# Kernel tuning notes

Measured on AMD Instinct MI355X. Metric: run time of the kernel, lower is better.

Reference implementation:

```python
import jax, jax.numpy as jnp
import numpy as np

N_NODES = 100000
N_EDGES = 800000
F_IN = 128
C_HID = 32
N_CLS = 16
K_HOPS = 3
CST = 1e-05


def setup_inputs() -> dict:
    key = jax.random.key(0)
    ks = jax.random.split(key, 12)
    node_feat = jax.random.normal(ks[0], (N_NODES, F_IN), dtype=jnp.float32)
    edge_index = jax.random.randint(ks[1], (2, N_EDGES), 0, N_NODES, dtype=jnp.int64)
    def lin(k, fan_in, fan_out):
        bound = 1.0 / np.sqrt(fan_in)
        kw, kb = jax.random.split(k)
        W = jax.random.uniform(kw, (fan_in, fan_out), minval=-bound, maxval=bound, dtype=jnp.float32)
        b = jax.random.uniform(kb, (fan_out,), minval=-bound, maxval=bound, dtype=jnp.float32)
        return W, b
    W_in, b_in = lin(ks[2], F_IN, C_HID)
    Wq, bq = lin(ks[3], C_HID, C_HID)
    Wk, bk = lin(ks[4], C_HID, C_HID)
    Wv, bv = lin(ks[5], C_HID, N_CLS)
    hopwise = jnp.ones((K_HOPS + 1,), dtype=jnp.float32)
    return {"node_feat": node_feat, "edge_index": edge_index,
            "W_in": W_in, "b_in": b_in, "Wq": Wq, "bq": bq,
            "Wk": Wk, "bk": bk, "Wv": Wv, "bv": bv, "hopwise": hopwise}


def reference(node_feat, edge_index, W_in, b_in, Wq, bq, Wk, bk, Wv, bv, hopwise):
    n = node_feat.shape[0]
    row, col = edge_index[0], edge_index[1]  # messages flow row -> col (PyG source_to_target)
    x = jax.nn.relu(node_feat @ W_in + b_in)            # [n, c]
    Q = 1.0 + jax.nn.elu(x @ Wq + bq)                    # [n, c]
    K = 1.0 + jax.nn.elu(x @ Wk + bk)                    # [n, c]
    V = x @ Wv + bv                                      # [n, d]
    M = jnp.einsum('ni,nj->nij', K, V)                   # [n, c, d]
    hidden = V * hopwise[0]
    for hop in range(K_HOPS):
        # scatter-sum aggregation over edges (aggr='add')
        M = jax.ops.segment_sum(M[row], col, num_segments=n)  # [n, c, d]
        K = jax.ops.segment_sum(K[row], col, num_segments=n)  # [n, c]
        H = jnp.einsum('ni,nij->nj', Q, M)               # [n, d]
        C = jnp.einsum('ni,ni->n', Q, K)[:, None] + CST  # [n, 1]
        hidden = hidden + hopwise[hop + 1] * (H / C)
    return hidden
```

## Files before the change

### kernel.cpp

```cpp
#include <hip/hip_runtime.h>
#include <math.h>

#define NN 100000
#define NE 800000
#define F_IN 128
#define CH 32
#define NC 16
#define CSTF 1e-5f
#define CAP 48

typedef float v2f __attribute__((ext_vector_type(2)));
typedef float v4f __attribute__((ext_vector_type(4)));
typedef short v8s __attribute__((ext_vector_type(8)));

__device__ __forceinline__ float bf_lo(unsigned int u) {
    unsigned int t = u << 16;
    return __builtin_bit_cast(float, t);
}
__device__ __forceinline__ float bf_hi(unsigned int u) {
    unsigned int t = u & 0xffff0000u;
    return __builtin_bit_cast(float, t);
}
__device__ __forceinline__ float bf_val(unsigned short v) {
    unsigned int t = ((unsigned int)v) << 16;
    return __builtin_bit_cast(float, t);
}
__device__ __forceinline__ v2f bf_pair(unsigned int u) {
    v2f r; r.x = bf_lo(u); r.y = bf_hi(u); return r;
}
__device__ __forceinline__ unsigned int bf_round(float a) {
    unsigned int ua = __builtin_bit_cast(unsigned int, a);
    return (ua + 0x7fffu + ((ua >> 16) & 1u)) >> 16;
}
__device__ __forceinline__ short bfq(float a) {
    unsigned int ua = __builtin_bit_cast(unsigned int, a);
    return (short)((ua + 0x8000u) >> 16);
}
__device__ __forceinline__ unsigned int bf_pack2(float a, float b) {
    return bf_round(a) | (bf_round(b) << 16);
}

__device__ __forceinline__ float cl448(float a) {
    return fminf(fmaxf(a, -448.f), 448.f);
}

__device__ __forceinline__ float elu1(float x) {
    return 1.f + ((x > 0.f) ? x : (expf(x) - 1.f));
}

__global__ void zero_kernel(int* __restrict__ p, int n) {
    int i = blockIdx.x * 256 + threadIdx.x;
    if (i < n) p[i] = 0;
}

__global__ void detect_kernel(const int* __restrict__ ei, int* __restrict__ mode) {
    __shared__ int any_nz;
    if (threadIdx.x == 0) any_nz = 0;
    __syncthreads();
    int nz = 0;
    for (int i = threadIdx.x; i < 4096; i += 256) nz |= (ei[2 * i + 1] != 0);
    if (nz) atomicOr(&any_nz, 1);
    __syncthreads();
    if (threadIdx.x == 0) *mode = any_nz ? 0 : 1;
}

__device__ __forceinline__ int get_row(const int* ei, int e, int m) {
    return m ? ei[2 * e] : ei[e];
}
__device__ __forceinline__ int get_col(const int* ei, int e, int m) {
    return m ? ei[2 * NE + 2 * e] : ei[NE + e];
}

__global__ void fillb_kernel(const int* __restrict__ ei, int* __restrict__ deg,
                             int* __restrict__ srcs, const int* __restrict__ mode) {
    int e = blockIdx.x * 256 + threadIdx.x;
    int m = *mode;
    if (e < NE) {
        int c = get_col(ei, e, m);
        int p = atomicAdd(&deg[c], 1);
        if (p < CAP) srcs[(size_t)c * CAP + p] = get_row(ei, e, m);
    }
}

__global__ __launch_bounds__(256) void phase1_kernel(
    const float* __restrict__ feat, const float* __restrict__ Win,
    const float* __restrict__ bin, const float* __restrict__ Wq,
    const float* __restrict__ bq, const float* __restrict__ Wk,
    const float* __restrict__ bk, const float* __restrict__ Wv,
    const float* __restrict__ bv, const float* __restrict__ hopwise,
    float* __restrict__ Qg, unsigned short* __restrict__ Kb,
    unsigned short* __restrict__ Vb, float* __restrict__ out)
{
    __shared__ float xs_all[4][16 * 36];

    int tid  = threadIdx.x;
    int wid  = tid >> 6;
    int lane = tid & 63;
    int q    = lane >> 4;
    int col  = lane & 15;
    int node0 = (blockIdx.x * 4 + wid) * 16;

    v8s wb[4][2];
#pragma unroll
    for (int kk = 0; kk < 4; ++kk)
#pragma unroll
        for (int t = 0; t < 2; ++t)
#pragma unroll
            for (int j = 0; j < 8; ++j)
                wb[kk][t][j] = (short)bf_round(Win[(kk * 32 + q * 8 + j) * CH + t * 16 + col]);

    v8s wq[2], wk[2], wv;
#pragma unroll
    for (int t = 0; t < 2; ++t)
#pragma unroll
        for (int j = 0; j < 8; ++j) {
            wq[t][j] = (short)bf_round(Wq[(q * 8 + j) * CH + t * 16 + col]);
            wk[t][j] = (short)bf_round(Wk[(q * 8 + j) * CH + t * 16 + col]);
        }
#pragma unroll
    for (int j = 0; j < 8; ++j)
        wv[j] = (short)bf_round(Wv[(q * 8 + j) * NC + col]);

    float bin0 = bin[col], bin1 = bin[col + 16];
    float bq0 = bq[col], bq1 = bq[col + 16];
    float bk0 = bk[col], bk1 = bk[col + 16];
    float bv0 = bv[col];
    float hw0 = hopwise[0];

    int nodeA = node0 + col;
    int nclamp = nodeA < NN ? nodeA : NN - 1;
    const float* fr = feat + (size_t)nclamp * F_IN + q * 8;

    v4f acc0 = {0.f, 0.f, 0.f, 0.f}, acc1 = {0.f, 0.f, 0.f, 0.f};
#pragma unroll
    for (int kk = 0; kk < 4; ++kk) {
        float4 a = *(const float4*)(fr + kk * 32);
        float4 b = *(const float4*)(fr + kk * 32 + 4);
        v8s af;
        af[0] = bfq(a.x); af[1] = bfq(a.y); af[2] = bfq(a.z); af[3] = bfq(a.w);
        af[4] = bfq(b.x); af[5] = bfq(b.y); af[6] = bfq(b.z); af[7] = bfq(b.w);
        acc0 = __builtin_amdgcn_mfma_f32_16x16x32_bf16(af, wb[kk][0], acc0, 0, 0, 0);
        acc1 = __builtin_amdgcn_mfma_f32_16x16x32_bf16(af, wb[kk][1], acc1, 0, 0, 0);
    }

    float* xs = xs_all[wid];
#pragma unroll
    for (int r = 0; r < 4; ++r) {
        xs[(q * 4 + r) * 36 + col]      = fmaxf(acc0[r] + bin0, 0.f);
        xs[(q * 4 + r) * 36 + col + 16] = fmaxf(acc1[r] + bin1, 0.f);
    }

    float4 xa = *(const float4*)&xs[col * 36 + q * 8];
    float4 xb = *(const float4*)&xs[col * 36 + q * 8 + 4];
    v8s xf;
    xf[0] = bfq(xa.x); xf[1] = bfq(xa.y); xf[2] = bfq(xa.z); xf[3] = bfq(xa.w);
    xf[4] = bfq(xb.x); xf[5] = bfq(xb.y); xf[6] = bfq(xb.z); xf[7] = bfq(xb.w);

    v4f aq0 = {0.f,0.f,0.f,0.f}, aq1 = {0.f,0.f,0.f,0.f};
    v4f ak0 = {0.f,0.f,0.f,0.f}, ak1 = {0.f,0.f,0.f,0.f};
    v4f av  = {0.f,0.f,0.f,0.f};
    aq0 = __builtin_amdgcn_mfma_f32_16x16x32_bf16(xf, wq[0], aq0, 0, 0, 0);
    aq1 = __builtin_amdgcn_mfma_f32_16x16x32_bf16(xf, wq[1], aq1, 0, 0, 0);
    ak0 = __builtin_amdgcn_mfma_f32_16x16x32_bf16(xf, wk[0], ak0, 0, 0, 0);
    ak1 = __builtin_amdgcn_mfma_f32_16x16x32_bf16(xf, wk[1], ak1, 0, 0, 0);
    av  = __builtin_amdgcn_mfma_f32_16x16x32_bf16(xf, wv,    av,  0, 0, 0);

#pragma unroll
    for (int r = 0; r < 4; ++r) {
        int nd = node0 + 4 * q + r;
        if (nd < NN) {
            float q0 = elu1(aq0[r] + bq0);
            float q1 = elu1(aq1[r] + bq1);
            float k0 = elu1(ak0[r] + bk0);
            float k1 = elu1(ak1[r] + bk1);
            float vv = av[r] + bv0;
            Qg[(size_t)nd * CH + col]      = q0;
            Qg[(size_t)nd * CH + col + 16] = q1;
            Kb[(size_t)nd * CH + col]      = (unsigned short)bf_round(k0);
            Kb[(size_t)nd * CH + col + 16] = (unsigned short)bf_round(k1);
            Vb[(size_t)nd * NC + col]      = (unsigned short)bf_round(vv);
            out[(size_t)nd * NC + col]     = hw0 * vv;
        }
    }
}

template<bool RANK1, bool WRITE>
__global__ __launch_bounds__(256) void hopB_kernel(
    const float* __restrict__ Qg, const unsigned short* __restrict__ Kb,
    const unsigned short* __restrict__ Vb, const unsigned char* __restrict__ Min,
    unsigned char* __restrict__ Mout, unsigned short* __restrict__ Kout,
    const int* __restrict__ deg, const int* __restrict__ srcs,
    const float* __restrict__ hopw, int hop, float* __restrict__ out)
{
    int tid  = threadIdx.x;
    int wid  = tid >> 6;
    int lane = tid & 63;
    int node = __builtin_amdgcn_readfirstlane(blockIdx.x * 4 + wid);
    int jB   = lane >> 2;
    int s4   = lane & 3;
    int cseg = s4 * 8;
    int c32  = lane & 31;

    v2f acc2[4];
#pragma unroll
    for (int t = 0; t < 4; ++t) { acc2[t].x = 0.f; acc2[t].y = 0.f; }
    v2f kagg2[4];
#pragma unroll
    for (int t = 0; t < 4; ++t) { kagg2[t].x = 0.f; kagg2[t].y = 0.f; }
    float kagg = 0.f;

    int d = deg[node];
    if (d > CAP) d = CAP;
    const int* sl = srcs + (size_t)node * CAP;
    int i = 0;

    if (RANK1) {
        for (; i + 3 < d; i += 4) {
            int s0 = sl[i], s1 = sl[i+1], s2 = sl[i+2], s3 = sl[i+3];
            uint4 kr0 = *(const uint4*)(Kb + (size_t)s0 * CH + cseg);
            uint4 kr1 = *(const uint4*)(Kb + (size_t)s1 * CH + cseg);
            uint4 kr2 = *(const uint4*)(Kb + (size_t)s2 * CH + cseg);
            uint4 kr3 = *(const uint4*)(Kb + (size_t)s3 * CH + cseg);
            float vj0 = bf_val(Vb[(size_t)s0 * NC + jB]);
            float vj1 = bf_val(Vb[(size_t)s1 * NC + jB]);
            float vj2 = bf_val(Vb[(size_t)s2 * NC + jB]);
            float vj3 = bf_val(Vb[(size_t)s3 * NC + jB]);
            v2f k;
            k = bf_pair(kr0.x); kagg2[0] += k; acc2[0] += k * vj0;
            k = bf_pair(kr0.y); kagg2[1] += k; acc2[1] += k * vj0;
            k = bf_pair(kr0.z); kagg2[2] += k; acc2[2] += k * vj0;
            k = bf_pair(kr0.w); kagg2[3] += k; acc2[3] += k * vj0;
            k = bf_pair(kr1.x); kagg2[0] += k; acc2[0] += k * vj1;
            k = bf_pair(kr1.y); kagg2[1] += k; acc2[1] += k * vj1;
            k = bf_pair(kr1.z); kagg2[2] += k; acc2[2] += k * vj1;
            k = bf_pair(kr1.w); kagg2[3] += k; acc2[3] += k * vj1;
            k = bf_pair(kr2.x); kagg2[0] += k; acc2[0] += k * vj2;
            k = bf_pair(kr2.y); kagg2[1] += k; acc2[1] += k * vj2;
            k = bf_pair(kr2.z); kagg2[2] += k; acc2[2] += k * vj2;
            k = bf_pair(kr2.w); kagg2[3] += k; acc2[3] += k * vj2;
            k = bf_pair(kr3.x); kagg2[0] += k; acc2[0] += k * vj3;
            k = bf_pair(kr3.y); kagg2[1] += k; acc2[1] += k * vj3;
            k = bf_pair(kr3.z); kagg2[2] += k; acc2[2] += k * vj3;
            k = bf_pair(kr3.w); kagg2[3] += k; acc2[3] += k * vj3;
        }
        for (; i < d; ++i) {
            int s0 = sl[i];
            uint4 kr0 = *(const uint4*)(Kb + (size_t)s0 * CH + cseg);
            float vj0 = bf_val(Vb[(size_t)s0 * NC + jB]);
            v2f k;
            k = bf_pair(kr0.x); kagg2[0] += k; acc2[0] += k * vj0;
            k = bf_pair(kr0.y); kagg2[1] += k; acc2[1] += k * vj0;
            k = bf_pair(kr0.z); kagg2[2] += k; acc2[2] += k * vj0;
            k = bf_pair(kr0.w); kagg2[3] += k; acc2[3] += k * vj0;
        }
    } else {
        for (; i + 3 < d; i += 4) {
            int s0 = sl[i], s1 = sl[i+1], s2 = sl[i+2], s3 = sl[i+3];
            uint2 u0 = *(const uint2*)(Min + (size_t)s0 * 512 + lane * 8);
            uint2 u1 = *(const uint2*)(Min + (size_t)s1 * 512 + lane * 8);
            uint2 u2 = *(const uint2*)(Min + (size_t)s2 * 512 + lane * 8);
            uint2 u3 = *(const uint2*)(Min + (size_t)s3 * 512 + lane * 8);
            float k0 = bf_val(Kb[(size_t)s0 * CH + c32]);
            float k1 = bf_val(Kb[(size_t)s1 * CH + c32]);
            float k2 = bf_val(Kb[(size_t)s2 * CH + c32]);
            float k3 = bf_val(Kb[(size_t)s3 * CH + c32]);
            kagg += (k0 + k1) + (k2 + k3);
            acc2[0] += (v2f)__builtin_amdgcn_cvt_pk_f32_fp8(u0.x, false);
            acc2[1] += (v2f)__builtin_amdgcn_cvt_pk_f32_fp8(u0.x, true);
            acc2[2] += (v2f)__builtin_amdgcn_cvt_pk_f32_fp8(u0.y, false);
            acc2[3] += (v2f)__builtin_amdgcn_cvt_pk_f32_fp8(u0.y, true);
            acc2[0] += (v2f)__builtin_amdgcn_cvt_pk_f32_fp8(u1.x, false);
            acc2[1] += (v2f)__builtin_amdgcn_cvt_pk_f32_fp8(u1.x, true);
            acc2[2] += (v2f)__builtin_amdgcn_cvt_pk_f32_fp8(u1.y, false);
            acc2[3] += (v2f)__builtin_amdgcn_cvt_pk_f32_fp8(u1.y, true);
            acc2[0] += (v2f)__builtin_amdgcn_cvt_pk_f32_fp8(u2.x, false);
            acc2[1] += (v2f)__builtin_amdgcn_cvt_pk_f32_fp8(u2.x, true);
            acc2[2] += (v2f)__builtin_amdgcn_cvt_pk_f32_fp8(u2.y, false);
            acc2[3] += (v2f)__builtin_amdgcn_cvt_pk_f32_fp8(u2.y, true);
            acc2[0] += (v2f)__builtin_amdgcn_cvt_pk_f32_fp8(u3.x, false);
            acc2[1] += (v2f)__builtin_amdgcn_cvt_pk_f32_fp8(u3.x, true);
            acc2[2] += (v2f)__builtin_amdgcn_cvt_pk_f32_fp8(u3.y, false);
            acc2[3] += (v2f)__builtin_amdgcn_cvt_pk_f32_fp8(u3.y, true);
        }
        for (; i < d; ++i) {
            int s0 = sl[i];
            uint2 u0 = *(const uint2*)(Min + (size_t)s0 * 512 + lane * 8);
            kagg += bf_val(Kb[(size_t)s0 * CH + c32]);
            acc2[0] += (v2f)__builtin_amdgcn_cvt_pk_f32_fp8(u0.x, false);
            acc2[1] += (v2f)__builtin_amdgcn_cvt_pk_f32_fp8(u0.x, true);
            acc2[2] += (v2f)__builtin_amdgcn_cvt_pk_f32_fp8(u0.y, false);
            acc2[3] += (v2f)__builtin_amdgcn_cvt_pk_f32_fp8(u0.y, true);
        }
    }

    const float4* qp = (const float4*)(Qg + (size_t)node * CH + cseg);
    float4 qa = qp[0], qb = qp[1];
    v2f q2[4];
    q2[0].x = qa.x; q2[0].y = qa.y; q2[1].x = qa.z; q2[1].y = qa.w;
    q2[2].x = qb.x; q2[2].y = qb.y; q2[3].x = qb.z; q2[3].y = qb.w;

    float cpv;
    if (RANK1) {
        v2f t = q2[0] * kagg2[0] + q2[1] * kagg2[1]
              + q2[2] * kagg2[2] + q2[3] * kagg2[3];
        cpv = t.x + t.y;
        cpv += __shfl_xor(cpv, 1);
        cpv += __shfl_xor(cpv, 2);
    } else {
        float qc = Qg[(size_t)node * CH + c32];
        cpv = qc * kagg;
#pragma unroll
        for (int st = 1; st <= 16; st <<= 1) cpv += __shfl_xor(cpv, st);
    }
    float sc = hopw[hop] / (cpv + CSTF);

    if (WRITE) {
        if (RANK1) {
            if (lane < 4) {
                uint4 kw;
                kw.x = bf_pack2(kagg2[0].x, kagg2[0].y);
                kw.y = bf_pack2(kagg2[1].x, kagg2[1].y);
                kw.z = bf_pack2(kagg2[2].x, kagg2[2].y);
                kw.w = bf_pack2(kagg2[3].x, kagg2[3].y);
                *(uint4*)(Kout + (size_t)node * CH + cseg) = kw;
            }
        } else {
            if (lane < 32)
                Kout[(size_t)node * CH + c32] = (unsigned short)bf_round(kagg);
        }
        int p0 = 0, p1 = 0;
        p0 = __builtin_amdgcn_cvt_pk_fp8_f32(cl448(acc2[0].x), cl448(acc2[0].y), p0, false);
        p0 = __builtin_amdgcn_cvt_pk_fp8_f32(cl448(acc2[1].x), cl448(acc2[1].y), p0, true);
        p1 = __builtin_amdgcn_cvt_pk_fp8_f32(cl448(acc2[2].x), cl448(acc2[2].y), p1, false);
        p1 = __builtin_amdgcn_cvt_pk_fp8_f32(cl448(acc2[3].x), cl448(acc2[3].y), p1, true);
        uint2 u; u.x = (unsigned int)p0; u.y = (unsigned int)p1;
        *(uint2*)(Mout + (size_t)node * 512 + lane * 8) = u;
    }

    v2f h2 = q2[0] * acc2[0] + q2[1] * acc2[1]
           + q2[2] * acc2[2] + q2[3] * acc2[3];
    float hp = h2.x + h2.y;
    hp += __shfl_xor(hp, 1);
    hp += __shfl_xor(hp, 2);

    if (s4 == 0)
        out[(size_t)node * NC + jB] += sc * hp;
}

extern "C" void kernel_launch(void* const* d_in, const int* in_sizes, int n_in,
                              void* d_out, int out_size, void* d_ws, size_t ws_size,
                              hipStream_t stream) {
    const float* feat = (const float*)d_in[0];
    const int*   ei   = (const int*)d_in[1];
    const float* Win  = (const float*)d_in[2];
    const float* bin  = (const float*)d_in[3];
    const float* Wq   = (const float*)d_in[4];
    const float* bq   = (const float*)d_in[5];
    const float* Wk   = (const float*)d_in[6];
    const float* bk   = (const float*)d_in[7];
    const float* Wv   = (const float*)d_in[8];
    const float* bv   = (const float*)d_in[9];
    const float* hopw = (const float*)d_in[10];
    float* out = (float*)d_out;

    char* ws = (char*)d_ws;
    size_t off = 0;
    auto alloc = [&](size_t bytes) -> void* {
        void* p = ws + off;
        off += (bytes + 255) & ~(size_t)255;
        return p;
    };
    float*          Qg  = (float*)alloc((size_t)NN * CH * 4);
    unsigned short* K0b = (unsigned short*)alloc((size_t)NN * CH * 2);
    unsigned short* K1b = (unsigned short*)alloc((size_t)NN * CH * 2);
    unsigned short* K2b = (unsigned short*)alloc((size_t)NN * CH * 2);
    unsigned short* Vb  = (unsigned short*)alloc((size_t)NN * NC * 2);
    int*   deg  = (int*)alloc((size_t)NN * 4);
    int*   mode = (int*)alloc(4);
    int*   srcs = (int*)alloc((size_t)NN * CAP * 4);
    unsigned char* MA = (unsigned char*)alloc((size_t)NN * 512);
    unsigned char* MB = (unsigned char*)alloc((size_t)NN * 512);

    zero_kernel<<<(NN + 255) / 256, 256, 0, stream>>>(deg, NN);
    detect_kernel<<<1, 256, 0, stream>>>(ei, mode);
    fillb_kernel<<<(NE + 255) / 256, 256, 0, stream>>>(ei, deg, srcs, mode);

    phase1_kernel<<<1563, 256, 0, stream>>>(feat, Win, bin, Wq, bq, Wk, bk, Wv, bv,
                                            hopw, Qg, K0b, Vb, out);

    hopB_kernel<true,  true ><<<25000, 256, 0, stream>>>(Qg, K0b, Vb, nullptr, MA, K1b, deg, srcs, hopw, 1, out);
    hopB_kernel<false, true ><<<25000, 256, 0, stream>>>(Qg, K1b, Vb, MA, MB, K2b, deg, srcs, hopw, 2, out);
    hopB_kernel<false, false><<<25000, 256, 0, stream>>>(Qg, K2b, Vb, MB, nullptr, nullptr, deg, srcs, hopw, 3, out);
}
```

Measured before the change: 392.4 us.

## Use persistent grid-stride hop kernels and fold mode detection into fill kernel

Hop kernels now launch a fixed 2048-block grid, and each wave walks nodes with a stride while prefetching the next node's degree and loading Q before the edge loop. The zero and detect kernels are removed: a memset clears the degrees and each fill block computes the index-layout mode itself with a wavefront ballot. The aim is to cut launch count and block scheduling overhead and to overlap metadata loads. The cost is fewer resident waves to hide gather latency, plus redundant mode detection work in every fill block.

```diff
diff --git a/kernel.cpp b/kernel.cpp
--- a/kernel.cpp
+++ b/kernel.cpp
@@ -8,6 +8,8 @@
 #define NC 16
 #define CSTF 1e-5f
 #define CAP 48
+#define PBLK 2048
+#define PSTRIDE (PBLK * 4)
 
 typedef float v2f __attribute__((ext_vector_type(2)));
 typedef float v4f __attribute__((ext_vector_type(4)));
@@ -48,22 +50,6 @@
     return 1.f + ((x > 0.f) ? x : (expf(x) - 1.f));
 }
 
-__global__ void zero_kernel(int* __restrict__ p, int n) {
-    int i = blockIdx.x * 256 + threadIdx.x;
-    if (i < n) p[i] = 0;
-}
-
-__global__ void detect_kernel(const int* __restrict__ ei, int* __restrict__ mode) {
-    __shared__ int any_nz;
-    if (threadIdx.x == 0) any_nz = 0;
-    __syncthreads();
-    int nz = 0;
-    for (int i = threadIdx.x; i < 4096; i += 256) nz |= (ei[2 * i + 1] != 0);
-    if (nz) atomicOr(&any_nz, 1);
-    __syncthreads();
-    if (threadIdx.x == 0) *mode = any_nz ? 0 : 1;
-}
-
 __device__ __forceinline__ int get_row(const int* ei, int e, int m) {
     return m ? ei[2 * e] : ei[e];
 }
@@ -72,9 +58,15 @@
 }
 
 __global__ void fillb_kernel(const int* __restrict__ ei, int* __restrict__ deg,
-                             int* __restrict__ srcs, const int* __restrict__ mode) {
+                             int* __restrict__ srcs) {
+    __shared__ int smode;
+    int nz = 0;
+    if (threadIdx.x < 64) nz = (ei[2 * threadIdx.x + 1] != 0) ? 1 : 0;
+    unsigned long long b = __ballot(nz);
+    if (threadIdx.x == 0) smode = (b == 0ULL) ? 1 : 0;
+    __syncthreads();
+    int m = smode;
     int e = blockIdx.x * 256 + threadIdx.x;
-    int m = *mode;
     if (e < NE) {
         int c = get_col(ei, e, m);
         int p = atomicAdd(&deg[c], 1);
@@ -184,37 +176,43 @@
     }
 }
 
-template<bool RANK1, bool WRITE>
-__global__ __launch_bounds__(256) void hopB_kernel(
+__global__ __launch_bounds__(256) void hopA_kernel(
     const float* __restrict__ Qg, const unsigned short* __restrict__ Kb,
-    const unsigned short* __restrict__ Vb, const unsigned char* __restrict__ Min,
+    const unsigned short* __restrict__ Vb,
     unsigned char* __restrict__ Mout, unsigned short* __restrict__ Kout,
     const int* __restrict__ deg, const int* __restrict__ srcs,
-    const float* __restrict__ hopw, int hop, float* __restrict__ out)
+    const float* __restrict__ hopw, float* __restrict__ out)
 {
     int tid  = threadIdx.x;
     int wid  = tid >> 6;
     int lane = tid & 63;
-    int node = __builtin_amdgcn_readfirstlane(blockIdx.x * 4 + wid);
     int jB   = lane >> 2;
     int s4   = lane & 3;
     int cseg = s4 * 8;
-    int c32  = lane & 31;
-
-    v2f acc2[4];
-#pragma unroll
-    for (int t = 0; t < 4; ++t) { acc2[t].x = 0.f; acc2[t].y = 0.f; }
-    v2f kagg2[4];
-#pragma unroll
-    for (int t = 0; t < 4; ++t) { kagg2[t].x = 0.f; kagg2[t].y = 0.f; }
-    float kagg = 0.f;
-
+    float hw = hopw[1];
+
+    int node = __builtin_amdgcn_readfirstlane(blockIdx.x * 4 + wid);
     int d = deg[node];
-    if (d > CAP) d = CAP;
-    const int* sl = srcs + (size_t)node * CAP;
-    int i = 0;
-
-    if (RANK1) {
+
+    while (true) {
+        int node_nx = node + PSTRIDE;
+        int d_nx = 0;
+        if (node_nx < NN) d_nx = deg[node_nx];
+
+        if (d > CAP) d = CAP;
+        const int* sl = srcs + (size_t)node * CAP;
+
+        const float4* qp = (const float4*)(Qg + (size_t)node * CH + cseg);
+        float4 qa = qp[0], qb = qp[1];
+
+        v2f acc2[4];
+#pragma unroll
+        for (int t = 0; t < 4; ++t) { acc2[t].x = 0.f; acc2[t].y = 0.f; }
+        v2f kagg2[4];
+#pragma unroll
+        for (int t = 0; t < 4; ++t) { kagg2[t].x = 0.f; kagg2[t].y = 0.f; }
+
+        int i = 0;
         for (; i + 3 < d; i += 4) {
             int s0 = sl[i], s1 = sl[i+1], s2 = sl[i+2], s3 = sl[i+3];
             uint4 kr0 = *(const uint4*)(Kb + (size_t)s0 * CH + cseg);
@@ -253,7 +251,87 @@
             k = bf_pair(kr0.z); kagg2[2] += k; acc2[2] += k * vj0;
             k = bf_pair(kr0.w); kagg2[3] += k; acc2[3] += k * vj0;
         }
-    } else {
+
+        v2f q2[4];
+        q2[0].x = qa.x; q2[0].y = qa.y; q2[1].x = qa.z; q2[1].y = qa.w;
+        q2[2].x = qb.x; q2[2].y = qb.y; q2[3].x = qb.z; q2[3].y = qb.w;
+
+        v2f t = q2[0] * kagg2[0] + q2[1] * kagg2[1]
+              + q2[2] * kagg2[2] + q2[3] * kagg2[3];
+        float cpv = t.x + t.y;
+        cpv += __shfl_xor(cpv, 1);
+        cpv += __shfl_xor(cpv, 2);
+        float sc = hw / (cpv + CSTF);
+
+        if (lane < 4) {
+            uint4 kw;
+            kw.x = bf_pack2(kagg2[0].x, kagg2[0].y);
+            kw.y = bf_pack2(kagg2[1].x, kagg2[1].y);
+            kw.z = bf_pack2(kagg2[2].x, kagg2[2].y);
+            kw.w = bf_pack2(kagg2[3].x, kagg2[3].y);
+            *(uint4*)(Kout + (size_t)node * CH + cseg) = kw;
+        }
+        int p0 = 0, p1 = 0;
+        p0 = __builtin_amdgcn_cvt_pk_fp8_f32(cl448(acc2[0].x), cl448(acc2[0].y), p0, false);
+        p0 = __builtin_amdgcn_cvt_pk_fp8_f32(cl448(acc2[1].x), cl448(acc2[1].y), p0, true);
+        p1 = __builtin_amdgcn_cvt_pk_fp8_f32(cl448(acc2[2].x), cl448(acc2[2].y), p1, false);
+        p1 = __builtin_amdgcn_cvt_pk_fp8_f32(cl448(acc2[3].x), cl448(acc2[3].y), p1, true);
+        uint2 u; u.x = (unsigned int)p0; u.y = (unsigned int)p1;
+        *(uint2*)(Mout + (size_t)node * 512 + lane * 8) = u;
+
+        v2f h2 = q2[0] * acc2[0] + q2[1] * acc2[1]
+               + q2[2] * acc2[2] + q2[3] * acc2[3];
+        float hp = h2.x + h2.y;
+        hp += __shfl_xor(hp, 1);
+        hp += __shfl_xor(hp, 2);
+
+        if (s4 == 0)
+            out[(size_t)node * NC + jB] += sc * hp;
+
+        if (node_nx >= NN) break;
+        node = node_nx;
+        d = d_nx;
+    }
+}
+
+template<bool WRITE>
+__global__ __launch_bounds__(256) void hopM_kernel(
+    const float* __restrict__ Qg, const unsigned short* __restrict__ Kb,
+    const unsigned char* __restrict__ Min,
+    unsigned char* __restrict__ Mout, unsigned short* __restrict__ Kout,
+    const int* __restrict__ deg, const int* __restrict__ srcs,
+    const float* __restrict__ hopw, int hop, float* __restrict__ out)
+{
+    int tid  = threadIdx.x;
+    int wid  = tid >> 6;
+    int lane = tid & 63;
+    int jB   = lane >> 2;
+    int s4   = lane & 3;
+    int cseg = s4 * 8;
+    int c32  = lane & 31;
+    float hw = hopw[hop];
+
+    int node = __builtin_amdgcn_readfirstlane(blockIdx.x * 4 + wid);
+    int d = deg[node];
+
+    while (true) {
+        int node_nx = node + PSTRIDE;
+        int d_nx = 0;
+        if (node_nx < NN) d_nx = deg[node_nx];
+
+        if (d > CAP) d = CAP;
+        const int* sl = srcs + (size_t)node * CAP;
+
+        float qcl = Qg[(size_t)node * CH + c32];
+        const float4* qp = (const float4*)(Qg + (size_t)node * CH + cseg);
+        float4 qa = qp[0], qb = qp[1];
+
+        v2f acc2[4];
+#pragma unroll
+        for (int t = 0; t < 4; ++t) { acc2[t].x = 0.f; acc2[t].y = 0.f; }
+        float kagg = 0.f;
+
+        int i = 0;
         for (; i + 3 < d; i += 4) {
             int s0 = sl[i], s1 = sl[i+1], s2 = sl[i+2], s3 = sl[i+3];
             uint2 u0 = *(const uint2*)(Min + (size_t)s0 * 512 + lane * 8);
@@ -291,60 +369,40 @@
             acc2[2] += (v2f)__builtin_amdgcn_cvt_pk_f32_fp8(u0.y, false);
             acc2[3] += (v2f)__builtin_amdgcn_cvt_pk_f32_fp8(u0.y, true);
         }
-    }
-
-    const float4* qp = (const float4*)(Qg + (size_t)node * CH + cseg);
-    float4 qa = qp[0], qb = qp[1];
-    v2f q2[4];
-    q2[0].x = qa.x; q2[0].y = qa.y; q2[1].x = qa.z; q2[1].y = qa.w;
-    q2[2].x = qb.x; q2[2].y = qb.y; q2[3].x = qb.z; q2[3].y = qb.w;
-
-    float cpv;
-    if (RANK1) {
-        v2f t = q2[0] * kagg2[0] + q2[1] * kagg2[1]
-              + q2[2] * kagg2[2] + q2[3] * kagg2[3];
-        cpv = t.x + t.y;
-        cpv += __shfl_xor(cpv, 1);
-        cpv += __shfl_xor(cpv, 2);
-    } else {
-        float qc = Qg[(size_t)node * CH + c32];
-        cpv = qc * kagg;
+
+        float cpv = qcl * kagg;
 #pragma unroll
         for (int st = 1; st <= 16; st <<= 1) cpv += __shfl_xor(cpv, st);
-    }
-    float sc = hopw[hop] / (cpv + CSTF);
-
-    if (WRITE) {
-        if (RANK1) {
-            if (lane < 4) {
-                uint4 kw;
-                kw.x = bf_pack2(kagg2[0].x, kagg2[0].y);
-                kw.y = bf_pack2(kagg2[1].x, kagg2[1].y);
-                kw.z = bf_pack2(kagg2[2].x, kagg2[2].y);
-                kw.w = bf_pack2(kagg2[3].x, kagg2[3].y);
-                *(uint4*)(Kout + (size_t)node * CH + cseg) = kw;
-            }
-        } else {
+        float sc = hw / (cpv + CSTF);
+
+        if (WRITE) {
             if (lane < 32)
                 Kout[(size_t)node * CH + c32] = (unsigned short)bf_round(kagg);
-        }
-        int p0 = 0, p1 = 0;
-        p0 = __builtin_amdgcn_cvt_pk_fp8_f32(cl448(acc2[0].x), cl448(acc2[0].y), p0, false);
-        p0 = __builtin_amdgcn_cvt_pk_fp8_f32(cl448(acc2[1].x), cl448(acc2[1].y), p0, true);
-        p1 = __builtin_amdgcn_cvt_pk_fp8_f32(cl448(acc2[2].x), cl448(acc2[2].y), p1, false);
-        p1 = __builtin_amdgcn_cvt_pk_fp8_f32(cl448(acc2[3].x), cl448(acc2[3].y), p1, true);
-        uint2 u; u.x = (unsigned int)p0; u.y = (unsigned int)p1;
-        *(uint2*)(Mout + (size_t)node * 512 + lane * 8) = u;
-    }
-
-    v2f h2 = q2[0] * acc2[0] + q2[1] * acc2[1]
-           + q2[2] * acc2[2] + q2[3] * acc2[3];
-    float hp = h2.x + h2.y;
-    hp += __shfl_xor(hp, 1);
-    hp += __shfl_xor(hp, 2);
-
-    if (s4 == 0)
-        out[(size_t)node * NC + jB] += sc * hp;
+            int p0 = 0, p1 = 0;
+            p0 = __builtin_amdgcn_cvt_pk_fp8_f32(cl448(acc2[0].x), cl448(acc2[0].y), p0, false);
+            p0 = __builtin_amdgcn_cvt_pk_fp8_f32(cl448(acc2[1].x), cl448(acc2[1].y), p0, true);
+            p1 = __builtin_amdgcn_cvt_pk_fp8_f32(cl448(acc2[2].x), cl448(acc2[2].y), p1, false);
+            p1 = __builtin_amdgcn_cvt_pk_fp8_f32(cl448(acc2[3].x), cl448(acc2[3].y), p1, true);
+            uint2 u; u.x = (unsigned int)p0; u.y = (unsigned int)p1;
+            *(uint2*)(Mout + (size_t)node * 512 + lane * 8) = u;
+        }
+
+        v2f q2[4];
+        q2[0].x = qa.x; q2[0].y = qa.y; q2[1].x = qa.z; q2[1].y = qa.w;
+        q2[2].x = qb.x; q2[2].y = qb.y; q2[3].x = qb.z; q2[3].y = qb.w;
+        v2f h2 = q2[0] * acc2[0] + q2[1] * acc2[1]
+               + q2[2] * acc2[2] + q2[3] * acc2[3];
+        float hp = h2.x + h2.y;
+        hp += __shfl_xor(hp, 1);
+        hp += __shfl_xor(hp, 2);
+
+        if (s4 == 0)
+            out[(size_t)node * NC + jB] += sc * hp;
+
+        if (node_nx >= NN) break;
+        node = node_nx;
+        d = d_nx;
+    }
 }
 
 extern "C" void kernel_launch(void* const* d_in, const int* in_sizes, int n_in,
@@ -376,19 +434,17 @@
     unsigned short* K2b = (unsigned short*)alloc((size_t)NN * CH * 2);
     unsigned short* Vb  = (unsigned short*)alloc((size_t)NN * NC * 2);
     int*   deg  = (int*)alloc((size_t)NN * 4);
-    int*   mode = (int*)alloc(4);
     int*   srcs = (int*)alloc((size_t)NN * CAP * 4);
     unsigned char* MA = (unsigned char*)alloc((size_t)NN * 512);
     unsigned char* MB = (unsigned char*)alloc((size_t)NN * 512);
 
-    zero_kernel<<<(NN + 255) / 256, 256, 0, stream>>>(deg, NN);
-    detect_kernel<<<1, 256, 0, stream>>>(ei, mode);
-    fillb_kernel<<<(NE + 255) / 256, 256, 0, stream>>>(ei, deg, srcs, mode);
+    hipMemsetAsync(deg, 0, (size_t)NN * 4, stream);
+    fillb_kernel<<<(NE + 255) / 256, 256, 0, stream>>>(ei, deg, srcs);
 
     phase1_kernel<<<1563, 256, 0, stream>>>(feat, Win, bin, Wq, bq, Wk, bk, Wv, bv,
                                             hopw, Qg, K0b, Vb, out);
 
-    hopB_kernel<true,  true ><<<25000, 256, 0, stream>>>(Qg, K0b, Vb, nullptr, MA, K1b, deg, srcs, hopw, 1, out);
-    hopB_kernel<false, true ><<<25000, 256, 0, stream>>>(Qg, K1b, Vb, MA, MB, K2b, deg, srcs, hopw, 2, out);
-    hopB_kernel<false, false><<<25000, 256, 0, stream>>>(Qg, K2b, Vb, MB, nullptr, nullptr, deg, srcs, hopw, 3, out);
-}
+    hopA_kernel<<<PBLK, 256, 0, stream>>>(Qg, K0b, Vb, MA, K1b, deg, srcs, hopw, out);
+    hopM_kernel<true ><<<PBLK, 256, 0, stream>>>(Qg, K1b, MA, MB, K2b, deg, srcs, hopw, 2, out);
+    hopM_kernel<false><<<PBLK, 256, 0, stream>>>(Qg, K2b, MB, nullptr, nullptr, deg, srcs, hopw, 3, out);
+}
```

Result: slower. 426.1 us (+8.6%).
